# Kernel tuning notes

Hardware: AMD Instinct MI355X
Metric: run time of the kernel (lower is better)

The kernel has to match this reference:

```python
import jax, jax.numpy as jnp
import numpy as np

B, S, D = 32, 1024, 1280          # batch, spatial tokens, hidden_size
CROSS = 768                        # cross_attention_dim
HEADS = 20
HD = D // HEADS                    # 64
N_AOE, N_IMG = 16, 16              # disease / anatomy token counts
SCALE = 1.0 / float(np.sqrt(HD))


def _split_heads(x):
    # [B, N, D] -> [B, H, N, HD]
    b, n, _ = x.shape
    return x.reshape(b, n, HEADS, HD).transpose(0, 2, 1, 3)


def _attend(q, k, v):
    # q: [B,H,S,HD], k/v: [B,H,K,HD]  (K is tiny, 16)
    scores = jnp.einsum('bhsd,bhkd->bhsk', q, k) * SCALE
    probs = jax.nn.softmax(scores, axis=-1)
    return jnp.einsum('bhsk,bhkd->bhsd', probs, v)


def setup_inputs() -> dict:
    key = jax.random.key(0)
    ks = jax.random.split(key, 10)
    g = lambda k, shape, sc=0.02: jax.random.normal(k, shape, jnp.float32) * sc
    return {
        'hidden_states': jax.random.normal(ks[0], (B, S, D), jnp.float32),
        'encoder_hidden_states': jax.random.normal(ks[1], (B, N_AOE + N_IMG + 16, CROSS), jnp.float32),
        'w_q': g(ks[2], (D, D)),            # attn.to_q, bias=False
        'w_k': g(ks[3], (D, CROSS)),        # attn.to_k (anatomy branch)
        'w_v': g(ks[4], (D, CROSS)),        # attn.to_v
        'w_k_dis': g(ks[5], (D, CROSS)),    # self.to_k_dis
        'w_v_dis': g(ks[6], (D, CROSS)),    # self.to_v_dis
        'w_gate': g(ks[7], (1, CROSS)),     # gate_modulator (randomized to exercise path; init is zeros)
        'b_gate': jnp.zeros((1,), jnp.float32),
        'anat_gate_logit': jnp.float32(0.0),  # logit(0.5) for block_type='both'
        'dis_gate_logit': jnp.float32(0.0),
        'w_out': g(ks[8], (D, D)),          # attn.to_out[0]
        'b_out': jnp.zeros((D,), jnp.float32),
    }


def reference(hidden_states, encoder_hidden_states, w_q, w_k, w_v, w_k_dis,
              w_v_dis, w_gate, b_gate, anat_gate_logit, dis_gate_logit,
              w_out, b_out):
    residual = hidden_states
    b = hidden_states.shape[0]

    # token splits (delta path disabled: delta_scale == 0.0)
    dis_tokens = encoder_hidden_states[:, :N_AOE, :]
    anat_tokens = encoder_hidden_states[:, N_AOE:N_AOE + N_IMG, :]

    # projections (torch Linear: x @ W^T)
    query = _split_heads(hidden_states @ w_q.T)          # [B,H,S,HD]
    k_anat = _split_heads(anat_tokens @ w_k.T)           # [B,H,16,HD]
    v_anat = _split_heads(anat_tokens @ w_v.T)
    k_dis = _split_heads(dis_tokens @ w_k_dis.T)
    v_dis = _split_heads(dis_tokens @ w_v_dis.T)

    z_anat = _attend(query, k_anat, v_anat)              # [B,H,S,HD]
    z_dis = _attend(query, k_dis, v_dis)

    # severity-driven gate shift
    severity = dis_tokens.mean(axis=1)                   # [B, CROSS]
    shift = (severity @ w_gate.T + b_gate).reshape(b, 1, 1, 1)
    anat_gate = jax.nn.sigmoid(anat_gate_logit - shift)
    dis_gate = jax.nn.sigmoid(dis_gate_logit + shift)

    z_final = anat_gate * z_anat + dis_gate * z_dis      # [B,H,S,HD]

    out = z_final.transpose(0, 2, 1, 3).reshape(b, -1, D)
    out = out @ w_out.T + b_out                          # to_out[0]; to_out[1] is dropout (eval identity)
    out = out + residual                                 # residual_connection=True, rescale_output_factor=1.0
    return out
```

## Files before the change

### kernel.cpp

```cpp
#include <hip/hip_runtime.h>
#include <stdint.h>

#define B_     32
#define S_     1024
#define D_     1280
#define CROSS_ 768
#define NTOK   16
#define SCALE_ 0.125f

typedef __bf16 bf16x8 __attribute__((ext_vector_type(8)));
typedef float  f32x4  __attribute__((ext_vector_type(4)));
typedef unsigned short ushort_t;
typedef unsigned int   uint_t;

__device__ __forceinline__ float b2f(ushort_t h){ return __uint_as_float(((uint_t)h)<<16); }
__device__ __forceinline__ ushort_t f2b(float f){
  uint_t u = __float_as_uint(f);
  u += 0x7FFFu + ((u>>16)&1u);
  return (ushort_t)(u>>16);
}
__device__ __forceinline__ uint_t pk2(float x, float y){
  return (uint_t)f2b(x) | ((uint_t)f2b(y)<<16);
}

__device__ __forceinline__ void gload_lds16(const void* g, void* l){
  __builtin_amdgcn_global_load_lds((const __attribute__((address_space(1))) void*)g,
                                   (__attribute__((address_space(3))) void*)l, 16, 0, 0);
}

__device__ __forceinline__ void decode_tile(int lin, int& m0, int& n0){
  int xcd = lin & 7, slot = lin >> 3;
  int m_tile = xcd + 8*(slot/10);
  int n_tile = slot - (slot/10)*10;
  m0 = m_tile*128; n0 = n_tile*128;
}

struct CvtArgs { const float* src[7]; ushort_t* dst[7]; int n[7]; };
__global__ void cvt_kernel(CvtArgs a){
  int t = blockIdx.y;
  const float* s = a.src[t]; ushort_t* d = a.dst[t]; int n = a.n[t];
  int i = (blockIdx.x*blockDim.x + threadIdx.x)*4;
  if(i >= n) return;
  float4 v = *(const float4*)(s+i);
  uint2 o; o.x = pk2(v.x,v.y); o.y = pk2(v.z,v.w);
  *(uint2*)(d+i) = o;
}

__global__ void cvt_big(const float* __restrict__ s, ushort_t* __restrict__ d, int n){
  int i = (blockIdx.x*blockDim.x + threadIdx.x)*8;
  if(i >= n) return;
  float4 v0 = *(const float4*)(s+i), v1 = *(const float4*)(s+i+4);
  uint4 o = { pk2(v0.x,v0.y), pk2(v0.z,v0.w), pk2(v1.x,v1.y), pk2(v1.z,v1.w) };
  *(uint4*)(d+i) = o;
}

__global__ void gates_kernel(const float* __restrict__ enc,
                             const float* __restrict__ w_gate,
                             const float* __restrict__ b_gate,
                             const float* __restrict__ aLog,
                             const float* __restrict__ dLog,
                             float* __restrict__ gates){
  int b = blockIdx.x, tid = threadIdx.x;
  __shared__ float red[256];
  float acc = 0.f;
  for(int k = tid; k < CROSS_; k += 256){
    float s = 0.f;
    for(int t = 0; t < NTOK; ++t)
      s += enc[(size_t)(b*48 + t)*CROSS_ + k];
    acc += w_gate[k] * s;
  }
  red[tid] = acc; __syncthreads();
  for(int off = 128; off > 0; off >>= 1){
    if(tid < off) red[tid] += red[tid+off];
    __syncthreads();
  }
  if(tid == 0){
    float shift = red[0]*(1.f/16.f) + b_gate[0];
    gates[b*2+0] = 1.f/(1.f+__expf(shift - aLog[0]));
    gates[b*2+1] = 1.f/(1.f+__expf(-(dLog[0] + shift)));
  }
}

__global__ __launch_bounds__(256) void kv_gemm(const ushort_t* __restrict__ enc,
      const ushort_t* __restrict__ wk,  const ushort_t* __restrict__ wv,
      const ushort_t* __restrict__ wkd, const ushort_t* __restrict__ wvd,
      ushort_t* __restrict__ kv){
  __shared__ __align__(16) ushort_t As[128*64];
  __shared__ __align__(16) ushort_t Bs[128*64];
  const int tau = blockIdx.z;
  const ushort_t* W = (tau==0)? wk : (tau==1)? wv : (tau==2)? wkd : wvd;
  const int tok_off = (tau < 2) ? NTOK : 0;
  const int m0 = blockIdx.x*128, n0 = blockIdx.y*128;
  const int tid = threadIdx.x, l = tid & 63, w = tid >> 6;
  const int wm = (w&1)*64, wn = (w>>1)*64;
  const f32x4 fz = {0.f,0.f,0.f,0.f};
  f32x4 acc[4][4];
  #pragma unroll
  for(int i=0;i<4;++i){
    #pragma unroll
    for(int j=0;j<4;++j) acc[i][j] = fz;
  }
  for(int kt = 0; kt < CROSS_/64; ++kt){
    const int k0 = kt*64;
    #pragma unroll
    for(int i=0;i<4;++i){
      int row = (w*4+i)*8 + (l>>3);
      int c   = l & 7;
      int gm  = m0 + row;
      int er  = (gm>>4)*48 + tok_off + (gm&15);
      gload_lds16(enc + (size_t)er*CROSS_ + k0 + c*8, As + (w*4+i)*512);
      gload_lds16(W  + (size_t)(n0+row)*CROSS_ + k0 + c*8, Bs + (w*4+i)*512);
    }
    __syncthreads();
    #pragma unroll
    for(int ks = 0; ks < 64; ks += 32){
      bf16x8 a[4], bq[4];
      #pragma unroll
      for(int i=0;i<4;++i) a[i]  = *(const bf16x8*)&As[(wm+i*16+(l&15))*64 + ks + (l>>4)*8];
      #pragma unroll
      for(int j=0;j<4;++j) bq[j] = *(const bf16x8*)&Bs[(wn+j*16+(l&15))*64 + ks + (l>>4)*8];
      #pragma unroll
      for(int i=0;i<4;++i){
        #pragma unroll
        for(int j=0;j<4;++j)
          acc[i][j] = __builtin_amdgcn_mfma_f32_16x16x32_bf16(a[i], bq[j], acc[i][j], 0,0,0);
      }
    }
    __syncthreads();
  }
  #pragma unroll
  for(int i=0;i<4;++i){
    #pragma unroll
    for(int j=0;j<4;++j){
      #pragma unroll
      for(int r=0;r<4;++r){
        int m = m0 + wm + i*16 + (l>>4)*4 + r;
        int n = n0 + wn + j*16 + (l&15);
        int b = m >> 4, t = m & 15;
        kv[(((size_t)tau*B_ + b)*NTOK + t)*D_ + n] = f2b(acc[i][j][r]);
      }
    }
  }
}

__global__ __launch_bounds__(256,3) void gemm1_attn(
      const ushort_t* __restrict__ X, const ushort_t* __restrict__ Wq,
      const ushort_t* __restrict__ kv, const float* __restrict__ gates,
      ushort_t* __restrict__ Z){
  __shared__ __align__(16) union {
    struct { ushort_t As[128*64]; ushort_t Bs[128*64]; } st;
    struct { union { ushort_t qs[128*132];
                     ushort_t ps[4][64*44]; } u;
             ushort_t ks[2*2*16*72];
             ushort_t vts[2*64*40]; } ep;
  } sm;
  int m0, n0; decode_tile(blockIdx.x, m0, n0);
  const int tid = threadIdx.x, l = tid & 63, w = tid >> 6;
  const int wm = (w&1)*64, wn = (w>>1)*64;
  const int b = m0 >> 10;
  const f32x4 fz = {0.f,0.f,0.f,0.f};
  f32x4 acc[4][4];
  #pragma unroll
  for(int i=0;i<4;++i){
    #pragma unroll
    for(int j=0;j<4;++j) acc[i][j] = fz;
  }
  for(int kt = 0; kt < D_/64; ++kt){
    const int k0 = kt*64;
    #pragma unroll
    for(int i=0;i<4;++i){
      int row = (w*4+i)*8 + (l>>3);
      int c   = l & 7;
      gload_lds16(X  + (size_t)(m0+row)*D_ + k0 + c*8, sm.st.As + (w*4+i)*512);
      gload_lds16(Wq + (size_t)(n0+row)*D_ + k0 + c*8, sm.st.Bs + (w*4+i)*512);
    }
    __syncthreads();
    #pragma unroll
    for(int ks = 0; ks < 64; ks += 32){
      bf16x8 a[4], bq[4];
      #pragma unroll
      for(int i=0;i<4;++i) a[i]  = *(const bf16x8*)&sm.st.As[(wm+i*16+(l&15))*64 + ks + (l>>4)*8];
      #pragma unroll
      for(int j=0;j<4;++j) bq[j] = *(const bf16x8*)&sm.st.Bs[(wn+j*16+(l&15))*64 + ks + (l>>4)*8];
      #pragma unroll
      for(int i=0;i<4;++i){
        #pragma unroll
        for(int j=0;j<4;++j)
          acc[i][j] = __builtin_amdgcn_mfma_f32_16x16x32_bf16(a[i], bq[j], acc[i][j], 0,0,0);
      }
    }
    __syncthreads();
  }
  #pragma unroll
  for(int i=0;i<4;++i){
    #pragma unroll
    for(int j=0;j<4;++j){
      #pragma unroll
      for(int r=0;r<4;++r)
        sm.ep.u.qs[(wm+i*16+(l>>4)*4+r)*132 + wn + j*16 + (l&15)] = f2b(acc[i][j][r]);
    }
  }
  for(int id = tid; id < 512; id += 256){
    int h  = id >> 8, rem = id & 255;
    int tk = rem >> 7, t = (rem>>3)&15, c = rem&7;
    int tensor = tk*2;
    const ushort_t* src = kv + (((size_t)tensor*B_ + b)*NTOK + t)*D_ + n0 + h*64 + c*8;
    *(uint4*)&sm.ep.ks[((h*2+tk)*16 + t)*72 + c*8] = *(const uint4*)src;
  }
  for(int id = tid; id < 512; id += 256){
    int h = id >> 8, rem = id & 255;
    int tp = rem >> 3, c = rem & 7;
    int tensor = (tp < 16) ? 1 : 3;
    int t = tp & 15;
    const ushort_t* src = kv + (((size_t)tensor*B_ + b)*NTOK + t)*D_ + n0 + h*64 + c*8;
    uint4 v = *(const uint4*)src;
    const ushort_t* pv = (const ushort_t*)&v;
    #pragma unroll
    for(int e=0;e<8;++e) sm.ep.vts[(h*64 + c*8 + e)*40 + tp] = pv[e];
  }
  __syncthreads();
  const int h = w >> 1, ws0 = (w&1)*64;
  const float gA = gates[b*2+0], gD = gates[b*2+1];
  f32x4 scA[4], scD[4];
  #pragma unroll
  for(int i=0;i<4;++i){ scA[i] = fz; scD[i] = fz; }
  #pragma unroll
  for(int ks0 = 0; ks0 < 64; ks0 += 32){
    bf16x8 qf[4];
    #pragma unroll
    for(int i=0;i<4;++i)
      qf[i] = *(const bf16x8*)&sm.ep.u.qs[(ws0+i*16+(l&15))*132 + h*64 + ks0 + (l>>4)*8];
    bf16x8 kA = *(const bf16x8*)&sm.ep.ks[((h*2+0)*16 + (l&15))*72 + ks0 + (l>>4)*8];
    bf16x8 kD = *(const bf16x8*)&sm.ep.ks[((h*2+1)*16 + (l&15))*72 + ks0 + (l>>4)*8];
    #pragma unroll
    for(int i=0;i<4;++i){
      scA[i] = __builtin_amdgcn_mfma_f32_16x16x32_bf16(qf[i], kA, scA[i], 0,0,0);
      scD[i] = __builtin_amdgcn_mfma_f32_16x16x32_bf16(qf[i], kD, scD[i], 0,0,0);
    }
  }
  __syncthreads();
  #pragma unroll
  for(int i=0;i<4;++i){
    #pragma unroll
    for(int r=0;r<4;++r){
      float vA = scA[i][r]*SCALE_, vD = scD[i][r]*SCALE_;
      float mA = vA, mD = vD;
      #pragma unroll
      for(int off=1; off<16; off<<=1){
        mA = fmaxf(mA, __shfl_xor(mA, off));
        mD = fmaxf(mD, __shfl_xor(mD, off));
      }
      float eA = __expf(vA - mA), eD = __expf(vD - mD);
      float sA = eA, sD = eD;
      #pragma unroll
      for(int off=1; off<16; off<<=1){
        sA += __shfl_xor(sA, off);
        sD += __shfl_xor(sD, off);
      }
      int lr = i*16 + (l>>4)*4 + r;
      sm.ep.u.ps[w][lr*44 + 0  + (l&15)] = f2b(gA*eA/sA);
      sm.ep.u.ps[w][lr*44 + 16 + (l&15)] = f2b(gD*eD/sD);
    }
  }
  f32x4 z[4][4];
  #pragma unroll
  for(int i=0;i<4;++i){
    #pragma unroll
    for(int j=0;j<4;++j) z[i][j] = fz;
  }
  bf16x8 pa[4], vb[4];
  #pragma unroll
  for(int i=0;i<4;++i) pa[i] = *(const bf16x8*)&sm.ep.u.ps[w][(i*16+(l&15))*44 + (l>>4)*8];
  #pragma unroll
  for(int j=0;j<4;++j) vb[j] = *(const bf16x8*)&sm.ep.vts[(h*64 + j*16 + (l&15))*40 + (l>>4)*8];
  #pragma unroll
  for(int i=0;i<4;++i){
    #pragma unroll
    for(int j=0;j<4;++j)
      z[i][j] = __builtin_amdgcn_mfma_f32_16x16x32_bf16(pa[i], vb[j], z[i][j], 0,0,0);
  }
  #pragma unroll
  for(int i=0;i<4;++i){
    #pragma unroll
    for(int j=0;j<4;++j){
      #pragma unroll
      for(int r=0;r<4;++r){
        int row = m0 + ws0 + i*16 + (l>>4)*4 + r;
        int col = n0 + h*64 + j*16 + (l&15);
        Z[(size_t)row*D_ + col] = f2b(z[i][j][r]);
      }
    }
  }
}

__global__ __launch_bounds__(256) void gemm2(
      const ushort_t* __restrict__ Zin, const ushort_t* __restrict__ Wo,
      const float* __restrict__ bias, const float* __restrict__ resid,
      float* __restrict__ out){
  __shared__ __align__(16) ushort_t As[128*64];
  __shared__ __align__(16) ushort_t Bs[128*64];
  int m0, n0; decode_tile(blockIdx.x, m0, n0);
  const int tid = threadIdx.x, l = tid & 63, w = tid >> 6;
  const int wm = (w&1)*64, wn = (w>>1)*64;
  const f32x4 fz = {0.f,0.f,0.f,0.f};
  f32x4 acc[4][4];
  #pragma unroll
  for(int i=0;i<4;++i){
    #pragma unroll
    for(int j=0;j<4;++j) acc[i][j] = fz;
  }
  for(int kt = 0; kt < D_/64; ++kt){
    const int k0 = kt*64;
    #pragma unroll
    for(int i=0;i<4;++i){
      int row = (w*4+i)*8 + (l>>3);
      int c   = l & 7;
      gload_lds16(Zin + (size_t)(m0+row)*D_ + k0 + c*8, As + (w*4+i)*512);
      gload_lds16(Wo  + (size_t)(n0+row)*D_ + k0 + c*8, Bs + (w*4+i)*512);
    }
    __syncthreads();
    #pragma unroll
    for(int ks = 0; ks < 64; ks += 32){
      bf16x8 a[4], bq[4];
      #pragma unroll
      for(int i=0;i<4;++i) a[i]  = *(const bf16x8*)&As[(wm+i*16+(l&15))*64 + ks + (l>>4)*8];
      #pragma unroll
      for(int j=0;j<4;++j) bq[j] = *(const bf16x8*)&Bs[(wn+j*16+(l&15))*64 + ks + (l>>4)*8];
      #pragma unroll
      for(int i=0;i<4;++i){
        #pragma unroll
        for(int j=0;j<4;++j)
          acc[i][j] = __builtin_amdgcn_mfma_f32_16x16x32_bf16(a[i], bq[j], acc[i][j], 0,0,0);
      }
    }
    __syncthreads();
  }
  float bj[4];
  #pragma unroll
  for(int j=0;j<4;++j) bj[j] = bias[n0 + wn + j*16 + (l&15)];
  #pragma unroll
  for(int i=0;i<4;++i){
    #pragma unroll
    for(int j=0;j<4;++j){
      #pragma unroll
      for(int r=0;r<4;++r){
        int m = m0 + wm + i*16 + (l>>4)*4 + r;
        int n = n0 + wn + j*16 + (l&15);
        out[(size_t)m*D_ + n] = acc[i][j][r] + bj[j] + resid[(size_t)m*D_ + n];
      }
    }
  }
}

extern "C" void kernel_launch(void* const* d_in, const int* in_sizes, int n_in,
                              void* d_out, int out_size, void* d_ws, size_t ws_size,
                              hipStream_t stream){
  const float* hidden = (const float*)d_in[0];
  const float* enc    = (const float*)d_in[1];
  const float* w_q    = (const float*)d_in[2];
  const float* w_k    = (const float*)d_in[3];
  const float* w_v    = (const float*)d_in[4];
  const float* w_kd   = (const float*)d_in[5];
  const float* w_vd   = (const float*)d_in[6];
  const float* w_gate = (const float*)d_in[7];
  const float* b_gate = (const float*)d_in[8];
  const float* aLog   = (const float*)d_in[9];
  const float* dLog   = (const float*)d_in[10];
  const float* w_out  = (const float*)d_in[11];
  const float* b_out  = (const float*)d_in[12];
  float* out = (float*)d_out;

  char* ws = (char*)d_ws;
  ushort_t* z_bf   = (ushort_t*)(ws + 0);
  ushort_t* kv_bf  = (ushort_t*)(ws + 83886080);
  ushort_t* wq_bf  = (ushort_t*)(ws + 89128960);
  ushort_t* wk_bf  = (ushort_t*)(ws + 92405760);
  ushort_t* wv_bf  = (ushort_t*)(ws + 94371840);
  ushort_t* wkd_bf = (ushort_t*)(ws + 96337920);
  ushort_t* wvd_bf = (ushort_t*)(ws + 98304000);
  ushort_t* wo_bf  = (ushort_t*)(ws + 100270080);
  ushort_t* enc_bf = (ushort_t*)(ws + 103546880);
  float*    gates  = (float*)   (ws + 105906176);

  ushort_t* hid_bf = (ushort_t*)d_out;

  CvtArgs ca;
  ca.src[0]=w_q;   ca.dst[0]=wq_bf;  ca.n[0]=D_*D_;
  ca.src[1]=w_k;   ca.dst[1]=wk_bf;  ca.n[1]=D_*CROSS_;
  ca.src[2]=w_v;   ca.dst[2]=wv_bf;  ca.n[2]=D_*CROSS_;
  ca.src[3]=w_kd;  ca.dst[3]=wkd_bf; ca.n[3]=D_*CROSS_;
  ca.src[4]=w_vd;  ca.dst[4]=wvd_bf; ca.n[4]=D_*CROSS_;
  ca.src[5]=w_out; ca.dst[5]=wo_bf;  ca.n[5]=D_*D_;
  ca.src[6]=enc;   ca.dst[6]=enc_bf; ca.n[6]=B_*48*CROSS_;
  cvt_kernel<<<dim3(1600,7), 256, 0, stream>>>(ca);
  cvt_big<<<20480, 256, 0, stream>>>(hidden, hid_bf, B_*S_*D_);

  gates_kernel<<<32, 256, 0, stream>>>(enc, w_gate, b_gate, aLog, dLog, gates);
  kv_gemm<<<dim3(4,10,4), 256, 0, stream>>>(enc_bf, wk_bf, wv_bf, wkd_bf, wvd_bf, kv_bf);
  gemm1_attn<<<2560, 256, 0, stream>>>(hid_bf, wq_bf, kv_bf, gates, z_bf);
  gemm2<<<2560, 256, 0, stream>>>(z_bf, wo_bf, b_out, hidden, out);
}
```

Baseline: 737.3 us.

## Rewrite output projection GEMM as 256x256 double-buffered 8-wave pipelined kernel

Replaces the 128x128-tile output GEMM with a 256x256-tile, 512-thread kernel. It double-buffers LDS, interleaves staged global-to-LDS loads with MFMA phases under explicit vmcnt waits and barriers, uses XOR-swizzled LDS layout to avoid bank conflicts, and remaps block IDs for L2 locality. It aims to hide memory latency and raise data reuse per tile. In exchange it uses 128KB of LDS and a 640-block grid, which may limit occupancy and leave the tail unbalanced.

```diff
diff --git a/kernel.cpp b/kernel.cpp
--- a/kernel.cpp
+++ b/kernel.cpp
@@ -293,63 +293,115 @@
   }
 }
 
-__global__ __launch_bounds__(256) void gemm2(
+#define VMW(n)  asm volatile("s_waitcnt vmcnt(" #n ")" ::: "memory")
+#define FENCE() asm volatile("" ::: "memory")
+#define BARX()  do{ FENCE(); __builtin_amdgcn_s_barrier(); FENCE(); }while(0)
+
+__device__ __forceinline__ void stage_aq(const ushort_t* __restrict__ g,
+                                         ushort_t* le, int tid){
+  int row = tid >> 3;
+  int c   = ((tid & 7) ^ (row & 7)) << 3;
+  gload_lds16(g + (size_t)row*D_ + c, le + (tid>>6)*512);
+}
+__device__ __forceinline__ void stage_b2(const ushort_t* __restrict__ g,
+                                         ushort_t* lh, int s0, int tid){
+  int w   = tid >> 6;
+  int blk = w >> 2;
+  int t   = tid & 255;
+  int rr  = s0 + blk*64 + (t >> 3);
+  int c   = ((t & 7) ^ (rr & 7)) << 3;
+  gload_lds16(g + (size_t)rr*D_ + c, lh + (s0 + blk*64)*64 + (w&3)*512);
+}
+
+__global__ __launch_bounds__(512,2) void gemm2_8p(
       const ushort_t* __restrict__ Zin, const ushort_t* __restrict__ Wo,
       const float* __restrict__ bias, const float* __restrict__ resid,
       float* __restrict__ out){
-  __shared__ __align__(16) ushort_t As[128*64];
-  __shared__ __align__(16) ushort_t Bs[128*64];
-  int m0, n0; decode_tile(blockIdx.x, m0, n0);
+  __shared__ __align__(16) ushort_t lds[65536];
+  const int lid = (blockIdx.x & 7)*80 + (blockIdx.x >> 3);
+  const int m0 = (lid/5)*256, n0 = (lid%5)*256;
   const int tid = threadIdx.x, l = tid & 63, w = tid >> 6;
-  const int wm = (w&1)*64, wn = (w>>1)*64;
+  const int wr = w >> 2, wc = w & 3;
+  const int lr = l & 15;
+  const int csw0 = ((l>>4)*8)      ^ ((l&7)<<3);
+  const int csw1 = (32+(l>>4)*8)   ^ ((l&7)<<3);
+  const int bro  = (wc & 1)*64 + lr;
+  const ushort_t* Asrc = Zin + (size_t)m0*D_;
+  const ushort_t* Bsrc = Wo  + (size_t)n0*D_;
   const f32x4 fz = {0.f,0.f,0.f,0.f};
-  f32x4 acc[4][4];
-  #pragma unroll
-  for(int i=0;i<4;++i){
+  f32x4 acc[8][4];
+  #pragma unroll
+  for(int i=0;i<8;++i){
     #pragma unroll
     for(int j=0;j<4;++j) acc[i][j] = fz;
   }
-  for(int kt = 0; kt < D_/64; ++kt){
-    const int k0 = kt*64;
-    #pragma unroll
-    for(int i=0;i<4;++i){
-      int row = (w*4+i)*8 + (l>>3);
-      int c   = l & 7;
-      gload_lds16(Zin + (size_t)(m0+row)*D_ + k0 + c*8, As + (w*4+i)*512);
-      gload_lds16(Wo  + (size_t)(n0+row)*D_ + k0 + c*8, Bs + (w*4+i)*512);
-    }
-    __syncthreads();
-    #pragma unroll
-    for(int ks = 0; ks < 64; ks += 32){
-      bf16x8 a[4], bq[4];
-      #pragma unroll
-      for(int i=0;i<4;++i) a[i]  = *(const bf16x8*)&As[(wm+i*16+(l&15))*64 + ks + (l>>4)*8];
-      #pragma unroll
-      for(int j=0;j<4;++j) bq[j] = *(const bf16x8*)&Bs[(wn+j*16+(l&15))*64 + ks + (l>>4)*8];
-      #pragma unroll
-      for(int i=0;i<4;++i){
-        #pragma unroll
-        for(int j=0;j<4;++j)
-          acc[i][j] = __builtin_amdgcn_mfma_f32_16x16x32_bf16(a[i], bq[j], acc[i][j], 0,0,0);
-      }
-    }
-    __syncthreads();
+  bf16x8 a[4][2], bb[2][2];
+
+#define AB(tt) (lds + ((tt)&1)*16384)
+#define BB(tt) (lds + 32768 + ((tt)&1)*16384)
+#define ST_S0(tt) { stage_aq(Asrc + (size_t)  0*D_ + (tt)*64, AB(tt),          tid); \
+                    stage_aq(Asrc + (size_t)128*D_ + (tt)*64, AB(tt) + 8192,   tid); }
+#define ST_S1(tt) { stage_b2(Bsrc + (size_t)  0*D_ + (tt)*64, BB(tt),        0, tid); \
+                    stage_b2(Bsrc + (size_t)128*D_ + (tt)*64, BB(tt) + 8192, 0, tid); }
+#define ST_S2(tt) { stage_b2(Bsrc + (size_t)  0*D_ + (tt)*64, BB(tt),       32, tid); \
+                    stage_b2(Bsrc + (size_t)128*D_ + (tt)*64, BB(tt) + 8192,32, tid); }
+#define ST_S3(tt) { stage_aq(Asrc + (size_t) 64*D_ + (tt)*64, AB(tt) + 4096,  tid); \
+                    stage_aq(Asrc + (size_t)192*D_ + (tt)*64, AB(tt) + 12288, tid); }
+#define DS_A(qi, Ab) { _Pragma("unroll") for(int i=0;i<4;++i){ \
+      a[i][0] = *(const bf16x8*)&(Ab)[((qi)*64 + i*16 + lr)*64 + csw0]; \
+      a[i][1] = *(const bf16x8*)&(Ab)[((qi)*64 + i*16 + lr)*64 + csw1]; } }
+#define DS_B(qj, Bb) { _Pragma("unroll") for(int j=0;j<2;++j){ \
+      bb[j][0] = *(const bf16x8*)&(Bb)[(bro + ((qj)*2+j)*16)*64 + csw0]; \
+      bb[j][1] = *(const bf16x8*)&(Bb)[(bro + ((qj)*2+j)*16)*64 + csw1]; } }
+#define MM(qi,qj) { __builtin_amdgcn_s_setprio(1); \
+    _Pragma("unroll") for(int i=0;i<4;++i){ _Pragma("unroll") for(int j=0;j<2;++j){ \
+      acc[(qi)*4+i][(qj)*2+j] = __builtin_amdgcn_mfma_f32_16x16x32_bf16(a[i][0], bb[j][0], acc[(qi)*4+i][(qj)*2+j],0,0,0); \
+      acc[(qi)*4+i][(qj)*2+j] = __builtin_amdgcn_mfma_f32_16x16x32_bf16(a[i][1], bb[j][1], acc[(qi)*4+i][(qj)*2+j],0,0,0); } } \
+    __builtin_amdgcn_s_setprio(0); }
+
+  ST_S0(0); ST_S1(0); ST_S2(0); ST_S3(0);
+  VMW(4);
+  BARX();
+  for(int t = 0; t < 19; ++t){
+    const ushort_t* Ab = AB(t) + wr*8192;
+    const ushort_t* Bb = BB(t) + (wc>>1)*8192;
+    DS_A(0,Ab); DS_B(0,Bb); ST_S0(t+1); VMW(4); BARX(); MM(0,0); BARX();
+    DS_B(1,Bb);             ST_S1(t+1); VMW(4); BARX(); MM(0,1); BARX();
+    DS_A(1,Ab); DS_B(0,Bb); ST_S2(t+1);         BARX(); MM(1,0); BARX();
+    DS_B(1,Bb);             ST_S3(t+1); VMW(4); BARX(); MM(1,1); BARX();
+  }
+  {
+    const ushort_t* Ab = AB(19) + wr*8192;
+    const ushort_t* Bb = BB(19) + (wc>>1)*8192;
+    DS_A(0,Ab); DS_B(0,Bb); VMW(2); BARX(); MM(0,0); BARX();
+    DS_B(1,Bb);             VMW(0); BARX(); MM(0,1); BARX();
+    DS_A(1,Ab); DS_B(0,Bb);         BARX(); MM(1,0); BARX();
+    DS_B(1,Bb);                             MM(1,1);
   }
   float bj[4];
   #pragma unroll
-  for(int j=0;j<4;++j) bj[j] = bias[n0 + wn + j*16 + (l&15)];
-  #pragma unroll
-  for(int i=0;i<4;++i){
+  for(int j=0;j<4;++j) bj[j] = bias[n0 + wc*64 + j*16 + lr];
+  #pragma unroll
+  for(int i=0;i<8;++i){
     #pragma unroll
     for(int j=0;j<4;++j){
       #pragma unroll
       for(int r=0;r<4;++r){
-        int m = m0 + wm + i*16 + (l>>4)*4 + r;
-        int n = n0 + wn + j*16 + (l&15);
+        int m = m0 + wr*128 + i*16 + (l>>4)*4 + r;
+        int n = n0 + wc*64 + j*16 + lr;
         out[(size_t)m*D_ + n] = acc[i][j][r] + bj[j] + resid[(size_t)m*D_ + n];
       }
     }
   }
+#undef AB
+#undef BB
+#undef ST_S0
+#undef ST_S1
+#undef ST_S2
+#undef ST_S3
+#undef DS_A
+#undef DS_B
+#undef MM
 }
 
 extern "C" void kernel_launch(void* const* d_in, const int* in_sizes, int n_in,
@@ -398,5 +450,5 @@
   gates_kernel<<<32, 256, 0, stream>>>(enc, w_gate, b_gate, aLog, dLog, gates);
   kv_gemm<<<dim3(4,10,4), 256, 0, stream>>>(enc_bf, wk_bf, wv_bf, wkd_bf, wvd_bf, kv_bf);
   gemm1_attn<<<2560, 256, 0, stream>>>(hid_bf, wq_bf, kv_bf, gates, z_bf);
-  gemm2<<<2560, 256, 0, stream>>>(z_bf, wo_bf, b_out, hidden, out);
-}
+  gemm2_8p<<<640, 512, 0, stream>>>(z_bf, wo_bf, b_out, hidden, out);
+}
```

After: 697.3 us. 5.4% less time.
